# Optimization experiments

Hardware: AMD Instinct MI355X
Metric: run time of the kernel (lower is better)

Reference implementation:

```python
import jax, jax.numpy as jnp
import numpy as np

B, N, K, D = 8, 32768, 128, 64
TAU, ITERS, EPS = 1.0, 10, 1e-8


def setup_inputs() -> dict:
    key = jax.random.key(0)
    k1, k2, k3 = jax.random.split(key, 3)
    xyz = jax.random.normal(k1, (B, 3, N), dtype=jnp.float32)
    feats = jax.random.normal(k2, (B, D, N), dtype=jnp.float32)
    o_scores = jax.random.uniform(k3, (B, N), dtype=jnp.float32)
    return {"xyz": xyz, "feats": feats, "o_scores": o_scores}


def _sq_dist(x, c):
    # x: (B,N,3), c: (B,K,3) -> (B,N,K) squared euclidean distance
    x2 = jnp.sum(x * x, axis=-1, keepdims=True)          # (B,N,1)
    c2 = jnp.sum(c * c, axis=-1)[:, None, :]              # (B,1,K)
    xc = jnp.einsum('bnd,bkd->bnk', x, c)                 # (B,N,K)
    return x2 + c2 - 2.0 * xc


def _wkeans_plus(x, f, s, n_clusters, iters, tau):
    # x: (B,N,3) points, f: (B,N,D) features, s: (B,N) soft weights
    n = x.shape[1]
    # deterministic init: evenly strided points as initial centroids
    init_idx = jnp.arange(n_clusters) * (n // n_clusters)
    centers = x[:, init_idx, :]                           # (B,K,3)
    w = s[..., None]                                      # (B,N,1)
    s_sum = jnp.sum(s, axis=1, keepdims=True) + EPS       # (B,1)
    gamma = None
    denom = None
    for _ in range(iters):
        d = _sq_dist(x, centers)                          # (B,N,K)
        gamma = jax.nn.softmax(-d / tau, axis=-1) * w     # (B,N,K) weighted soft assignment
        denom = jnp.sum(gamma, axis=1) + EPS              # (B,K)
        centers = jnp.einsum('bnk,bnd->bkd', gamma, x) / denom[..., None]
    pi = jnp.sum(gamma, axis=1) / s_sum                   # (B,K) mixing weights
    node_feats = jnp.einsum('bnk,bnd->bkd', gamma, f) / denom[..., None]  # (B,K,D)
    return gamma, pi, centers, node_feats


def reference(xyz, feats, o_scores):
    x = jnp.swapaxes(xyz, -1, -2)    # (B,N,3)
    f = jnp.swapaxes(feats, -1, -2)  # (B,N,D)
    gamma, pi, node_xyz, node_feats = _wkeans_plus(x, f, o_scores, K, ITERS, TAU)
    return gamma, pi, node_xyz, node_feats
```

## Files before the change

kernel.cpp:

```cpp
#include <hip/hip_runtime.h>
#include <hip/hip_bf16.h>

typedef __attribute__((ext_vector_type(8))) short short8;
typedef __attribute__((ext_vector_type(4))) float f32x4;

#define BB 8
#define NN 32768
#define KK 128
#define DD 64
#define TAU 1.0f
#define ITERS 10
#define EPSV 1e-8f
#define JPARTS 128

#define G_SZ   ((size_t)BB * NN * KK)
#define PI_OFF (G_SZ)
#define XY_OFF (PI_OFF + (size_t)BB * KK)
#define NF_OUT (XY_OFF + (size_t)BB * KK * 3)

#define SLICE_F (BB * KK * 4)
#define HDR_F   ((ITERS + 1) * SLICE_F)

__device__ __forceinline__ unsigned pk2(float a, float b) {
    __hip_bfloat162 h = __float22bfloat162_rn(make_float2(a, b));
    unsigned u; __builtin_memcpy(&u, &h, 4); return u;
}

template <bool FIRST, bool LAST>
__global__ __launch_bounds__(256) void assign_kernel(
    const float* __restrict__ xyz, const float* __restrict__ sc,
    const float4* __restrict__ accIn,
    float* __restrict__ accOut,
    float* __restrict__ gamma_out)
{
    __shared__ float4 cLds[KK];
    __shared__ float4 wLds[512];
    __shared__ float  accW[4][512];

    const int b = blockIdx.y, blk = blockIdx.x;
    const int tid = threadIdx.x, wave = tid >> 6, lane = tid & 63;

    const float* X = xyz + (size_t)b * 3 * NN;
    const float* S = sc + (size_t)b * NN;

    const int n = blk * 512 + tid;
    const float px0 = X[n],       py0 = X[NN + n],       pz0 = X[2 * NN + n],       ps0 = S[n];
    const float px1 = X[n + 256], py1 = X[NN + n + 256], pz1 = X[2 * NN + n + 256], ps1 = S[n + 256];

    if (tid < KK) {
        float cx, cy, cz;
        if (FIRST) {
            int i0 = tid * (NN / KK);
            cx = X[i0]; cy = X[NN + i0]; cz = X[2 * NN + i0];
        } else {
            float4 a = accIn[b * KK + tid];
            float denom = a.w + EPSV;
            cx = a.x / denom; cy = a.y / denom; cz = a.z / denom;
        }
        cLds[tid] = make_float4(2.f * cx / TAU, 2.f * cy / TAU, 2.f * cz / TAU,
                                -(cx * cx + cy * cy + cz * cz) / TAU);
    }
    __syncthreads();

    float l0a = 0.f, l0b = 0.f, l1a = 0.f, l1b = 0.f;
    #pragma unroll 8
    for (int k = 0; k < KK; k += 2) {
        float4 ca = cLds[k], cb = cLds[k + 1];
        l0a += __expf(fmaf(px0, ca.x, fmaf(py0, ca.y, fmaf(pz0, ca.z, ca.w))));
        l1a += __expf(fmaf(px1, ca.x, fmaf(py1, ca.y, fmaf(pz1, ca.z, ca.w))));
        l0b += __expf(fmaf(px0, cb.x, fmaf(py0, cb.y, fmaf(pz0, cb.z, cb.w))));
        l1b += __expf(fmaf(px1, cb.x, fmaf(py1, cb.y, fmaf(pz1, cb.z, cb.w))));
    }
    wLds[tid]       = make_float4(px0, py0, pz0, ps0 / (l0a + l0b));
    wLds[tid + 256] = make_float4(px1, py1, pz1, ps1 / (l1a + l1b));
    __syncthreads();

    const float4 c0 = cLds[lane];
    const float4 c1 = cLds[lane + 64];
    float ax0 = 0, ay0 = 0, az0 = 0, aw0 = 0;
    float ax1 = 0, ay1 = 0, az1 = 0, aw1 = 0;
    float* grow = gamma_out + ((size_t)b * NN + blk * 512 + (wave << 7)) * KK + lane;

    #pragma unroll 4
    for (int j = 0; j < 128; ++j) {
        float4 P = wLds[(wave << 7) | j];
        float g0 = __expf(fmaf(P.x, c0.x, fmaf(P.y, c0.y, fmaf(P.z, c0.z, c0.w)))) * P.w;
        float g1 = __expf(fmaf(P.x, c1.x, fmaf(P.y, c1.y, fmaf(P.z, c1.z, c1.w)))) * P.w;
        if (LAST) {
            grow[(size_t)j * KK] = g0;
            grow[(size_t)j * KK + 64] = g1;
        }
        ax0 = fmaf(g0, P.x, ax0); ay0 = fmaf(g0, P.y, ay0);
        az0 = fmaf(g0, P.z, az0); aw0 += g0;
        ax1 = fmaf(g1, P.x, ax1); ay1 = fmaf(g1, P.y, ay1);
        az1 = fmaf(g1, P.z, az1); aw1 += g1;
    }

    ((float4*)accW[wave])[lane]      = make_float4(ax0, ay0, az0, aw0);
    ((float4*)accW[wave])[lane + 64] = make_float4(ax1, ay1, az1, aw1);
    __syncthreads();
    float v0 = accW[0][tid]       + accW[1][tid]       + accW[2][tid]       + accW[3][tid];
    float v1 = accW[0][tid + 256] + accW[1][tid + 256] + accW[2][tid + 256] + accW[3][tid + 256];
    float* ag = accOut + b * (KK * 4);
    atomicAdd(ag + tid, v0);
    atomicAdd(ag + tid + 256, v1);
}

__global__ __launch_bounds__(256) void final_kernel(const float* __restrict__ sc,
                                                    const float* __restrict__ ws,
                                                    float* __restrict__ out) {
    int b = blockIdx.x, tid = threadIdx.x, wave = tid >> 6, lane = tid & 63;
    const float* S = sc + (size_t)b * NN;
    float sum = 0.f;
    for (int i = tid; i < NN; i += 256) sum += S[i];
    #pragma unroll
    for (int m = 1; m <= 32; m <<= 1) sum += __shfl_xor(sum, m, 64);
    __shared__ float red[4];
    if (lane == 0) red[wave] = sum;
    __syncthreads();
    if (tid < KK) {
        float ssum = red[0] + red[1] + red[2] + red[3] + EPSV;
        float4 a = ((const float4*)(ws + ITERS * SLICE_F))[b * KK + tid];
        float denom = a.w + EPSV;
        float* oxyz = out + XY_OFF + (size_t)(b * KK + tid) * 3;
        oxyz[0] = a.x / denom; oxyz[1] = a.y / denom; oxyz[2] = a.z / denom;
        out[PI_OFF + b * KK + tid] = a.w / ssum;
    }
}

__global__ __launch_bounds__(256) void nf_mfma2(const float* __restrict__ gamma,
                                                const float* __restrict__ feats,
                                                float* __restrict__ nf_acc) {
    __shared__ unsigned short gT[KK * 40];
    const int b = blockIdx.y, part = blockIdx.x;
    const int tid = threadIdx.x, wave = tid >> 6, lane = tid & 63;
    const int r = lane & 15, hi = lane >> 4;
    const int p = tid & 15, q0 = tid >> 4;

    f32x4 acc[2][4];
    #pragma unroll
    for (int kt = 0; kt < 2; kt++)
        #pragma unroll
        for (int dt = 0; dt < 4; dt++) acc[kt][dt] = (f32x4){0.f, 0.f, 0.f, 0.f};

    const float* gb = gamma + (size_t)b * NN * KK + (size_t)part * 256 * KK;
    const float* fb = feats + (size_t)b * DD * NN;
    const int n0 = part * 256;

    for (int ch = 0; ch < 8; ++ch) {
        const float* gr0 = gb + (size_t)(ch * 32 + 2 * p) * KK;
        const float* gr1 = gr0 + KK;
        unsigned* rowd = (unsigned*)gT;
        #pragma unroll
        for (int s = 0; s < 2; ++s) {
            int q = q0 + 16 * s;
            float4 x = *(const float4*)(gr0 + 4 * q);
            float4 y = *(const float4*)(gr1 + 4 * q);
            rowd[(4 * q + 0) * 20 + p] = pk2(x.x, y.x);
            rowd[(4 * q + 1) * 20 + p] = pk2(x.y, y.y);
            rowd[(4 * q + 2) * 20 + p] = pk2(x.z, y.z);
            rowd[(4 * q + 3) * 20 + p] = pk2(x.w, y.w);
        }
        __syncthreads();

        const unsigned short* a0p = gT + (wave * 32 + r) * 40 + hi * 8;
        short8 a0 = *(const short8*)a0p;
        short8 a1 = *(const short8*)(a0p + 16 * 40);
        const int nn = n0 + ch * 32 + hi * 8;
        #pragma unroll
        for (int dt = 0; dt < 4; ++dt) {
            const float* fr = fb + (size_t)(dt * 16 + r) * NN + nn;
            float4 x = *(const float4*)fr;
            float4 y = *(const float4*)(fr + 4);
            union { unsigned u[4]; short8 s; } bu;
            bu.u[0] = pk2(x.x, x.y); bu.u[1] = pk2(x.z, x.w);
            bu.u[2] = pk2(y.x, y.y); bu.u[3] = pk2(y.z, y.w);
            acc[0][dt] = __builtin_amdgcn_mfma_f32_16x16x32_bf16(a0, bu.s, acc[0][dt], 0, 0, 0);
            acc[1][dt] = __builtin_amdgcn_mfma_f32_16x16x32_bf16(a1, bu.s, acc[1][dt], 0, 0, 0);
        }
        __syncthreads();
    }

    float* nf = nf_acc + (size_t)b * KK * DD + (size_t)(wave * 32) * DD;
    #pragma unroll
    for (int kt = 0; kt < 2; kt++)
        #pragma unroll
        for (int dt = 0; dt < 4; dt++)
            #pragma unroll
            for (int rr = 0; rr < 4; rr++)
                atomicAdd(&nf[(kt * 16 + hi * 4 + rr) * DD + dt * 16 + r],
                          acc[kt][dt][rr]);
}

__global__ __launch_bounds__(256) void nf_finalize(const float* __restrict__ ws,
                                                   float* __restrict__ out) {
    int idx = blockIdx.x * 256 + threadIdx.x;
    int bk = idx / DD;
    float denom = ws[ITERS * SLICE_F + bk * 4 + 3] + EPSV;
    out[NF_OUT + idx] = out[NF_OUT + idx] / denom;
}

extern "C" void kernel_launch(void* const* d_in, const int* in_sizes, int n_in,
                              void* d_out, int out_size, void* d_ws, size_t ws_size,
                              hipStream_t stream) {
    const float* xyz = (const float*)d_in[0];
    const float* feats = (const float*)d_in[1];
    const float* sc = (const float*)d_in[2];
    float* out = (float*)d_out;
    float* ws = (float*)d_ws;

    hipMemsetAsync(ws, 0, (size_t)HDR_F * sizeof(float), stream);
    hipMemsetAsync(out + NF_OUT, 0, (size_t)BB * KK * DD * sizeof(float), stream);

    assign_kernel<true, false><<<dim3(64, BB), 256, 0, stream>>>(
        xyz, sc, nullptr, ws + SLICE_F, out);
    for (int it = 1; it < ITERS - 1; it++) {
        assign_kernel<false, false><<<dim3(64, BB), 256, 0, stream>>>(
            xyz, sc, (const float4*)(ws + it * SLICE_F),
            ws + (it + 1) * SLICE_F, out);
    }
    assign_kernel<false, true><<<dim3(64, BB), 256, 0, stream>>>(
        xyz, sc, (const float4*)(ws + (ITERS - 1) * SLICE_F),
        ws + ITERS * SLICE_F, out);

    final_kernel<<<BB, 256, 0, stream>>>(sc, ws, out);
    nf_mfma2<<<dim3(JPARTS, BB), 256, 0, stream>>>(out, feats, out + NF_OUT);
    nf_finalize<<<256, 256, 0, stream>>>(ws, out);
}
```

Baseline: 294.8 us.

## Compute softmax normalizer via wave DPP reduction instead of separate exp pass

Removes the first pass where each thread computed 128 exponentials per point to get the softmax denominator. Each wave now computes the exponentials for its 128 clusters once per point (two per lane), sums them across the wave with DPP row shifts, row broadcasts and a readlane, then normalizes. This halves the exp work and removes one LDS centroid table and one barrier. In exchange it adds cross-lane reduction latency per point and switches to an approximate divide.

After: 334.8 us. 1.14x slower.

```diff
diff --git a/kernel.cpp b/kernel.cpp
--- a/kernel.cpp
+++ b/kernel.cpp
@@ -25,6 +25,14 @@
     __hip_bfloat162 h = __float22bfloat162_rn(make_float2(a, b));
     unsigned u; __builtin_memcpy(&u, &h, 4); return u;
 }
+__device__ __forceinline__ float rdl(float v, int l) {
+    return __int_as_float(__builtin_amdgcn_readlane(__float_as_int(v), l));
+}
+template <int CTRL, int RMASK>
+__device__ __forceinline__ float dpp_add(float x) {
+    int t = __builtin_amdgcn_update_dpp(0, __float_as_int(x), CTRL, RMASK, 0xf, false);
+    return x + __int_as_float(t);
+}
 
 template <bool FIRST, bool LAST>
 __global__ __launch_bounds__(256) void assign_kernel(
@@ -33,7 +41,6 @@
     float* __restrict__ accOut,
     float* __restrict__ gamma_out)
 {
-    __shared__ float4 cLds[KK];
     __shared__ float4 wLds[512];
     __shared__ float  accW[4][512];
 
@@ -44,56 +51,71 @@
     const float* S = sc + (size_t)b * NN;
 
     const int n = blk * 512 + tid;
-    const float px0 = X[n],       py0 = X[NN + n],       pz0 = X[2 * NN + n],       ps0 = S[n];
-    const float px1 = X[n + 256], py1 = X[NN + n + 256], pz1 = X[2 * NN + n + 256], ps1 = S[n + 256];
-
-    if (tid < KK) {
-        float cx, cy, cz;
-        if (FIRST) {
-            int i0 = tid * (NN / KK);
-            cx = X[i0]; cy = X[NN + i0]; cz = X[2 * NN + i0];
-        } else {
-            float4 a = accIn[b * KK + tid];
-            float denom = a.w + EPSV;
-            cx = a.x / denom; cy = a.y / denom; cz = a.z / denom;
-        }
-        cLds[tid] = make_float4(2.f * cx / TAU, 2.f * cy / TAU, 2.f * cz / TAU,
-                                -(cx * cx + cy * cy + cz * cz) / TAU);
-    }
+    wLds[tid]       = make_float4(X[n], X[NN + n], X[2 * NN + n], S[n]);
+    wLds[tid + 256] = make_float4(X[n + 256], X[NN + n + 256], X[2 * NN + n + 256], S[n + 256]);
+
+    float cx0, cy0, cz0, cx1, cy1, cz1;
+    if (FIRST) {
+        const int i0 = lane * (NN / KK), i1 = (lane + 64) * (NN / KK);
+        cx0 = X[i0]; cy0 = X[NN + i0]; cz0 = X[2 * NN + i0];
+        cx1 = X[i1]; cy1 = X[NN + i1]; cz1 = X[2 * NN + i1];
+    } else {
+        float4 a0 = accIn[b * KK + lane];
+        float4 a1 = accIn[b * KK + 64 + lane];
+        float d0 = a0.w + EPSV, d1 = a1.w + EPSV;
+        cx0 = a0.x / d0; cy0 = a0.y / d0; cz0 = a0.z / d0;
+        cx1 = a1.x / d1; cy1 = a1.y / d1; cz1 = a1.z / d1;
+    }
+    const float4 c0 = make_float4(2.f * cx0 / TAU, 2.f * cy0 / TAU, 2.f * cz0 / TAU,
+                                  -(cx0 * cx0 + cy0 * cy0 + cz0 * cz0) / TAU);
+    const float4 c1 = make_float4(2.f * cx1 / TAU, 2.f * cy1 / TAU, 2.f * cz1 / TAU,
+                                  -(cx1 * cx1 + cy1 * cy1 + cz1 * cz1) / TAU);
     __syncthreads();
 
-    float l0a = 0.f, l0b = 0.f, l1a = 0.f, l1b = 0.f;
-    #pragma unroll 8
-    for (int k = 0; k < KK; k += 2) {
-        float4 ca = cLds[k], cb = cLds[k + 1];
-        l0a += __expf(fmaf(px0, ca.x, fmaf(py0, ca.y, fmaf(pz0, ca.z, ca.w))));
-        l1a += __expf(fmaf(px1, ca.x, fmaf(py1, ca.y, fmaf(pz1, ca.z, ca.w))));
-        l0b += __expf(fmaf(px0, cb.x, fmaf(py0, cb.y, fmaf(pz0, cb.z, cb.w))));
-        l1b += __expf(fmaf(px1, cb.x, fmaf(py1, cb.y, fmaf(pz1, cb.z, cb.w))));
-    }
-    wLds[tid]       = make_float4(px0, py0, pz0, ps0 / (l0a + l0b));
-    wLds[tid + 256] = make_float4(px1, py1, pz1, ps1 / (l1a + l1b));
-    __syncthreads();
-
-    const float4 c0 = cLds[lane];
-    const float4 c1 = cLds[lane + 64];
     float ax0 = 0, ay0 = 0, az0 = 0, aw0 = 0;
     float ax1 = 0, ay1 = 0, az1 = 0, aw1 = 0;
     float* grow = gamma_out + ((size_t)b * NN + blk * 512 + (wave << 7)) * KK + lane;
 
-    #pragma unroll 4
-    for (int j = 0; j < 128; ++j) {
-        float4 P = wLds[(wave << 7) | j];
-        float g0 = __expf(fmaf(P.x, c0.x, fmaf(P.y, c0.y, fmaf(P.z, c0.z, c0.w)))) * P.w;
-        float g1 = __expf(fmaf(P.x, c1.x, fmaf(P.y, c1.y, fmaf(P.z, c1.z, c1.w)))) * P.w;
-        if (LAST) {
-            grow[(size_t)j * KK] = g0;
-            grow[(size_t)j * KK + 64] = g1;
-        }
-        ax0 = fmaf(g0, P.x, ax0); ay0 = fmaf(g0, P.y, ay0);
-        az0 = fmaf(g0, P.z, az0); aw0 += g0;
-        ax1 = fmaf(g1, P.x, ax1); ay1 = fmaf(g1, P.y, ay1);
-        az1 = fmaf(g1, P.z, az1); aw1 += g1;
+    for (int jc = 0; jc < 16; ++jc) {
+        float4 P[8];
+        #pragma unroll
+        for (int u = 0; u < 8; ++u) P[u] = wLds[(wave << 7) | (jc * 8 + u)];
+
+        float e0[8], e1[8], l[8];
+        #pragma unroll
+        for (int u = 0; u < 8; ++u) {
+            e0[u] = __expf(fmaf(P[u].x, c0.x, fmaf(P[u].y, c0.y, fmaf(P[u].z, c0.z, c0.w))));
+            e1[u] = __expf(fmaf(P[u].x, c1.x, fmaf(P[u].y, c1.y, fmaf(P[u].z, c1.z, c1.w))));
+            l[u] = e0[u] + e1[u];
+        }
+        #pragma unroll
+        for (int u = 0; u < 8; ++u) l[u] = dpp_add<0x111, 0xf>(l[u]);
+        #pragma unroll
+        for (int u = 0; u < 8; ++u) l[u] = dpp_add<0x112, 0xf>(l[u]);
+        #pragma unroll
+        for (int u = 0; u < 8; ++u) l[u] = dpp_add<0x114, 0xf>(l[u]);
+        #pragma unroll
+        for (int u = 0; u < 8; ++u) l[u] = dpp_add<0x118, 0xf>(l[u]);
+        #pragma unroll
+        for (int u = 0; u < 8; ++u) l[u] = dpp_add<0x142, 0xa>(l[u]);
+        #pragma unroll
+        for (int u = 0; u < 8; ++u) l[u] = dpp_add<0x143, 0xc>(l[u]);
+        #pragma unroll
+        for (int u = 0; u < 8; ++u) l[u] = rdl(l[u], 63);
+
+        #pragma unroll
+        for (int u = 0; u < 8; ++u) {
+            float w = __fdividef(P[u].w, l[u]);
+            float g0 = e0[u] * w, g1 = e1[u] * w;
+            if (LAST) {
+                grow[(size_t)(jc * 8 + u) * KK] = g0;
+                grow[(size_t)(jc * 8 + u) * KK + 64] = g1;
+            }
+            ax0 = fmaf(g0, P[u].x, ax0); ay0 = fmaf(g0, P[u].y, ay0);
+            az0 = fmaf(g0, P[u].z, az0); aw0 += g0;
+            ax1 = fmaf(g1, P[u].x, ax1); ay1 = fmaf(g1, P[u].y, ay1);
+            az1 = fmaf(g1, P[u].z, az1); aw1 += g1;
+        }
     }
 
     ((float4*)accW[wave])[lane]      = make_float4(ax0, ay0, az0, aw0);
```
